# Performance work log

Measured on AMD Instinct MI355X. Metric: run time of the kernel, lower is better.

The kernel has to match this reference:

```python
import jax, jax.numpy as jnp
import numpy as np

B, T, C = 2, 4096, 768
N_HEAD = 12
HEAD_DIM = C // N_HEAD


def setup_inputs() -> dict:
    key = jax.random.key(0)
    k1, k2, k3, k4, k5 = jax.random.split(key, 5)
    scale = 1.0 / np.sqrt(C)
    x = jax.random.normal(k1, (B, T, C), dtype=jnp.float32)
    # weights stored as [in, out] (transpose of torch Linear weight)
    W_attn = jax.random.normal(k2, (C, 3 * C), dtype=jnp.float32) * scale
    b_attn = jax.random.normal(k3, (3 * C,), dtype=jnp.float32) * 0.01
    W_proj = jax.random.normal(k4, (C, C), dtype=jnp.float32) * scale
    b_proj = jax.random.normal(k5, (C,), dtype=jnp.float32) * 0.01
    return {"x": x, "W_attn": W_attn, "b_attn": b_attn, "W_proj": W_proj, "b_proj": b_proj}


def reference(x, W_attn, b_attn, W_proj, b_proj):
    Bq, Tq, Cq = x.shape
    qkv = x @ W_attn + b_attn                      # [B, T, 3C]
    q, k, v = jnp.split(qkv, 3, axis=-1)           # each [B, T, C]

    def heads(t):
        return t.reshape(Bq, Tq, N_HEAD, HEAD_DIM).transpose(0, 2, 1, 3)  # [B, H, T, D]

    q, k, v = heads(q), heads(k), heads(v)
    att = jnp.einsum('bhqd,bhkd->bhqk', q, k) * (1.0 / np.sqrt(HEAD_DIM))  # [B, H, T, T]
    causal = jnp.tril(jnp.ones((Tq, Tq), dtype=bool))                      # [T, T]
    att = jnp.where(causal[None, None], att, jnp.finfo(att.dtype).min)
    att = jax.nn.softmax(att, axis=-1)
    y = jnp.einsum('bhqk,bhkd->bhqd', att, v)      # [B, H, T, D]
    y = y.transpose(0, 2, 1, 3).reshape(Bq, Tq, Cq)
    return y @ W_proj + b_proj
```

## Files before the change

kernel.cpp:

```cpp
#include <hip/hip_runtime.h>


#define TSEQ   4096
#define NHEAD  12
#define CDIM   768
#define C3     2304
#define BT_TOT 8192

typedef __bf16 bf16x8 __attribute__((ext_vector_type(8)));
typedef __bf16 bf16x2 __attribute__((ext_vector_type(2)));
typedef float  f32x4  __attribute__((ext_vector_type(4)));
typedef unsigned int u32x4 __attribute__((ext_vector_type(4)));

__device__ __forceinline__ unsigned short f2bf(float f) {
  unsigned int u = __builtin_bit_cast(unsigned int, f);
  u += 0x7FFFu + ((u >> 16) & 1u);
  return (unsigned short)(u >> 16);
}

__device__ __forceinline__ unsigned int pack2bf(float a, float b) {
  bf16x2 v = {(__bf16)a, (__bf16)b};
  return __builtin_bit_cast(unsigned int, v);
}

__device__ __forceinline__ f32x4 mfma16(bf16x8 a, bf16x8 b, f32x4 c) {
  return __builtin_amdgcn_mfma_f32_16x16x32_bf16(a, b, c, 0, 0, 0);
}

typedef const __attribute__((address_space(1))) void* gas_ptr;
typedef __attribute__((address_space(3))) void* las_ptr;

#define WAIT_VM4() __builtin_amdgcn_s_waitcnt(0x3F74)
#define WAIT_VM0() __builtin_amdgcn_s_waitcnt(0x3F70)
#define SBAR()     __builtin_amdgcn_sched_barrier(0)


#define PREP_CAST_BLOCKS  6144
#define PREP_WA_BLOCKS    1728
#define PREP_WP_BLOCKS     576

__global__ __launch_bounds__(256) void prep_kernel(
    const float* __restrict__ x, unsigned short* __restrict__ xb,
    const float* __restrict__ W_attn, unsigned short* __restrict__ WaT,
    const float* __restrict__ W_proj, unsigned short* __restrict__ WpT) {
  const int bk = blockIdx.x;
  if (bk < PREP_CAST_BLOCKS) {
    int i = (bk * 256 + threadIdx.x) * 4;
    float4 v = *(const float4*)(x + i);
    ushort4 u;
    u.x = f2bf(v.x); u.y = f2bf(v.y); u.z = f2bf(v.z); u.w = f2bf(v.w);
    *(ushort4*)(xb + i) = u;
    return;
  }
  __shared__ float tile[32][33];
  const float* src;
  unsigned short* dst;
  int K, N, n0, k0;
  if (bk < PREP_CAST_BLOCKS + PREP_WA_BLOCKS) {
    const int j = bk - PREP_CAST_BLOCKS;
    src = W_attn; dst = WaT; K = CDIM; N = C3;
    n0 = (j % 72) * 32; k0 = (j / 72) * 32;
  } else {
    const int j = bk - (PREP_CAST_BLOCKS + PREP_WA_BLOCKS);
    src = W_proj; dst = WpT; K = CDIM; N = CDIM;
    n0 = (j % 24) * 32; k0 = (j / 24) * 32;
  }
  const int tx = threadIdx.x & 31, ty = threadIdx.x >> 5;
#pragma unroll
  for (int i = 0; i < 4; ++i)
    tile[ty + i * 8][tx] = src[(size_t)(k0 + ty + i * 8) * N + n0 + tx];
  __syncthreads();
#pragma unroll
  for (int i = 0; i < 4; ++i)
    dst[(size_t)(n0 + ty + i * 8) * K + k0 + tx] = f2bf(tile[tx][ty + i * 8]);
}


__device__ __forceinline__ void stage_gemm(const unsigned short* __restrict__ A,
                                           const unsigned short* __restrict__ BTm,
                                           int K, int m0, int n0, int k0,
                                           unsigned short* buf, int wave,
                                           int srow, int scol) {
#pragma unroll
  for (int r = 0; r < 2; ++r) {
    const unsigned short* ga = A + (size_t)(m0 + r * 64 + srow) * K + k0 + scol;
    __builtin_amdgcn_global_load_lds((gas_ptr)ga,
        (las_ptr)(buf + r * 2048 + wave * 512), 16, 0, 0);
    const unsigned short* gb = BTm + (size_t)(n0 + r * 64 + srow) * K + k0 + scol;
    __builtin_amdgcn_global_load_lds((gas_ptr)gb,
        (las_ptr)(buf + 4096 + r * 2048 + wave * 512), 16, 0, 0);
  }
}

__device__ __forceinline__ void gemm_bt_mainloop(const unsigned short* __restrict__ A,
                                                 const unsigned short* __restrict__ BTm,
                                                 int K, int m0, int n0,
                                                 unsigned short* lds, f32x4 acc[4][4]) {
  const int tid = threadIdx.x;
  const int wave = tid >> 6, lane = tid & 63;
  const int quad = lane >> 4, l16 = lane & 15;
  const int wm = (wave >> 1) * 64, wn = (wave & 1) * 64;
  const int srow = tid >> 2;
  const int scol = (tid & 3) * 8;

  const int nt = K / 32;
  stage_gemm(A, BTm, K, m0, n0, 0,  lds,        wave, srow, scol);
  stage_gemm(A, BTm, K, m0, n0, 32, lds + 8192, wave, srow, scol);
  WAIT_VM4();
  SBAR();
  __builtin_amdgcn_s_barrier();
  SBAR();

  for (int t = 0; t < nt; ++t) {
    if (t + 2 < nt) {
      stage_gemm(A, BTm, K, m0, n0, (t + 2) * 32, lds + ((t + 2) % 3) * 8192,
                 wave, srow, scol);
      WAIT_VM4();
    } else {
      WAIT_VM0();
    }
    SBAR();

    const unsigned short* buf = lds + (t % 3) * 8192;
    bf16x8 af[4], bfr[4];
#pragma unroll
    for (int i = 0; i < 4; ++i) {
      af[i]  = *(const bf16x8*)(buf + (wm + i * 16 + l16) * 32 + quad * 8);
      bfr[i] = *(const bf16x8*)(buf + 4096 + (wn + i * 16 + l16) * 32 + quad * 8);
    }
#pragma unroll
    for (int i = 0; i < 4; ++i)
#pragma unroll
      for (int j = 0; j < 4; ++j)
        acc[i][j] = mfma16(af[i], bfr[j], acc[i][j]);

    if (t + 1 < nt) {
      SBAR();
      __builtin_amdgcn_s_barrier();
      SBAR();
    }
  }
  __syncthreads();
}

__global__ __launch_bounds__(256, 3) void gemm_qkv_kernel(
    const unsigned short* __restrict__ A, const unsigned short* __restrict__ BTm,
    const float* __restrict__ bias,
    unsigned short* __restrict__ qbuf, unsigned short* __restrict__ kbuf,
    unsigned short* __restrict__ vtbuf) {
  __shared__ __align__(16) unsigned short lds[3 * 8192];
  f32x4 zero = {0.f, 0.f, 0.f, 0.f};
  f32x4 acc[4][4];
#pragma unroll
  for (int i = 0; i < 4; ++i)
#pragma unroll
    for (int j = 0; j < 4; ++j) acc[i][j] = zero;

  const int m0 = blockIdx.y * 128, n0 = blockIdx.x * 128;
  gemm_bt_mainloop(A, BTm, CDIM, m0, n0, lds, acc);

  const int tid = threadIdx.x;
  const int wave = tid >> 6, lane = tid & 63;
  const int quad = lane >> 4, l16 = lane & 15;
  const int wm = (wave >> 1) * 64, wn = (wave & 1) * 64;
  const float KSCALE = 0.125f * 1.44269504088896340736f;

  const int seg = n0 / CDIM;
  const float mult = (seg == 1) ? KSCALE : 1.0f;

#pragma unroll
  for (int j = 0; j < 4; ++j) {
    const int nl = wn + j * 16 + l16;
    const float bv = bias[n0 + nl];
#pragma unroll
    for (int i = 0; i < 4; ++i) {
#pragma unroll
      for (int r = 0; r < 4; ++r) {
        const int ml = wm + i * 16 + quad * 4 + r;
        unsigned short val = f2bf((acc[i][j][r] + bv) * mult);
        if (seg < 2) lds[ml * 136 + nl] = val;
        else         lds[nl * 136 + ml] = val;
      }
    }
  }
  __syncthreads();

  const int row = tid >> 1, half = tid & 1;
  const unsigned short* src = lds + row * 136 + half * 64;
  if (seg < 2) {
    const int m = m0 + row, b = m >> 12, t = m & (TSEQ - 1);
    const int nn = (n0 - seg * CDIM) + half * 64;
    const int h = nn >> 6;
    unsigned short* base = (seg == 0) ? qbuf : kbuf;
    unsigned short* dst = base + ((size_t)(b * NHEAD + h) * TSEQ + t) * 64;
#pragma unroll
    for (int k = 0; k < 8; ++k)
      *(uint4*)(dst + k * 8) = *(const uint4*)(src + k * 8);
  } else {
    const int nn = (n0 - 2 * CDIM) + row;
    const int h = nn >> 6, d = nn & 63;
    const int b = m0 >> 12, t0 = (m0 & (TSEQ - 1)) + half * 64;
    unsigned short* dst = vtbuf + ((size_t)(b * NHEAD + h) * 64 + d) * TSEQ + t0;
#pragma unroll
    for (int k = 0; k < 8; ++k) {
      const int s0 = 32 * (k >> 2) + 4 * (k & 3);
      uint2 a = *(const uint2*)(src + s0);
      uint2 c = *(const uint2*)(src + s0 + 16);
      uint4 w = {a.x, a.y, c.x, c.y};
      *(uint4*)(dst + k * 8) = w;
    }
  }
}

__global__ __launch_bounds__(256, 3) void gemm_out_kernel(
    const unsigned short* __restrict__ A, const unsigned short* __restrict__ BTm,
    const float* __restrict__ bias, float* __restrict__ out) {
  __shared__ __align__(16) unsigned short lds[3 * 8192];
  f32x4 zero = {0.f, 0.f, 0.f, 0.f};
  f32x4 acc[4][4];
#pragma unroll
  for (int i = 0; i < 4; ++i)
#pragma unroll
    for (int j = 0; j < 4; ++j) acc[i][j] = zero;

  const int m0 = blockIdx.y * 128, n0 = blockIdx.x * 128;
  gemm_bt_mainloop(A, BTm, CDIM, m0, n0, lds, acc);

  const int tid = threadIdx.x;
  const int wave = tid >> 6, lane = tid & 63;
  const int quad = lane >> 4, l16 = lane & 15;
  const int wm = (wave >> 1) * 64, wn = (wave & 1) * 64;

#pragma unroll
  for (int j = 0; j < 4; ++j) {
    int n = n0 + wn + j * 16 + l16;
    float bv = bias[n];
#pragma unroll
    for (int i = 0; i < 4; ++i) {
#pragma unroll
      for (int r = 0; r < 4; ++r) {
        int m = m0 + wm + i * 16 + quad * 4 + r;
        out[(size_t)m * CDIM + n] = acc[i][j][r] + bv;
      }
    }
  }
}


__device__ __forceinline__ void stage_kv(const unsigned short* __restrict__ Kp,
                                         const unsigned short* __restrict__ Vp,
                                         int j0, unsigned short* kb, unsigned short* vb,
                                         int tid, int wave) {
  const int row = tid >> 3;
  const int col = ((tid & 7) ^ (row & 7)) * 8;
  __builtin_amdgcn_global_load_lds((gas_ptr)(Kp + (size_t)(j0 + row) * 64 + col),
                                   (las_ptr)(kb + wave * 512), 16, 0, 0);
  __builtin_amdgcn_global_load_lds((gas_ptr)(Vp + (size_t)row * TSEQ + j0 + col),
                                   (las_ptr)(vb + wave * 512), 16, 0, 0);
}

__device__ __forceinline__ void qk_score(const bf16x8 kf[8], const bf16x8 qf[2], f32x4 s[4]) {
  f32x4 zero = {0.f, 0.f, 0.f, 0.f};
#pragma unroll
  for (int i = 0; i < 4; ++i)
    s[i] = mfma16(kf[2 * i + 1], qf[1], mfma16(kf[2 * i], qf[0], zero));
}

template <bool MASKED>
__device__ __forceinline__ void exp_pack(const f32x4 s[4], int j0, int qabs,
                                         int l16, int quad, float& lsum, bf16x8 pf[2]) {
  unsigned int w[8];
#pragma unroll
  for (int i = 0; i < 4; ++i) {
    float p[4];
#pragma unroll
    for (int r = 0; r < 4; ++r) {
      p[r] = __builtin_amdgcn_exp2f(s[i][r]);
      if (MASKED) {
        if (j0 + i * 16 + quad * 4 + r > qabs) p[r] = 0.f;
      }
      lsum += p[r];
    }
    w[2 * i]     = pack2bf(p[0], p[1]);
    w[2 * i + 1] = pack2bf(p[2], p[3]);
  }
  u32x4 lo = {w[0], w[1], w[2], w[3]};
  u32x4 hi = {w[4], w[5], w[6], w[7]};
  pf[0] = __builtin_bit_cast(bf16x8, lo);
  pf[1] = __builtin_bit_cast(bf16x8, hi);
}

__device__ __forceinline__ void pv(const unsigned short* __restrict__ vb,
                                   int l16, int quad, int x7,
                                   const bf16x8 pf[2], f32x4 o[4]) {
#pragma unroll
  for (int dt = 0; dt < 4; ++dt) {
    const unsigned short* vr = vb + (dt * 16 + l16) * 64;
    bf16x8 v0 = *(const bf16x8*)(vr + ((quad ^ x7) * 8));
    bf16x8 v1 = *(const bf16x8*)(vr + (((4 + quad) ^ x7) * 8));
    o[dt] = mfma16(v1, pf[1], mfma16(v0, pf[0], o[dt]));
  }
}

__global__ __launch_bounds__(512, 6) void attn_kernel(const unsigned short* __restrict__ qbuf,
                                                      const unsigned short* __restrict__ kbuf,
                                                      const unsigned short* __restrict__ vtbuf,
                                                      unsigned short* __restrict__ y) {
  __shared__ __align__(16) unsigned short k_lds[2][64 * 64];
  __shared__ __align__(16) unsigned short v_lds[2][64 * 64];

  const int tid = threadIdx.x;
  const int wave = tid >> 6, lane = tid & 63;
  const int quad = lane >> 4, l16 = lane & 15;
  const int x7 = l16 & 7;

  const int bh = blockIdx.x % 24;
  const int p = blockIdx.x / 24;
  const bool isA = wave < 4;
  const int qtile = isA ? p : (63 - p);
  const int q0 = qtile * 64 + (wave & 3) * 16;

  const unsigned short* Qp = qbuf + (size_t)bh * TSEQ * 64;
  const unsigned short* Kp = kbuf + (size_t)bh * TSEQ * 64;
  const unsigned short* Vp = vtbuf + (size_t)bh * 64 * TSEQ;

  bf16x8 qf[2];
  qf[0] = *(const bf16x8*)(Qp + (size_t)(q0 + l16) * 64 + quad * 8);
  qf[1] = *(const bf16x8*)(Qp + (size_t)(q0 + l16) * 64 + 32 + quad * 8);

  f32x4 zero = {0.f, 0.f, 0.f, 0.f};
  f32x4 o[4];
#pragma unroll
  for (int dt = 0; dt < 4; ++dt) o[dt] = zero;
  float ls = 0.f;

  const int kcol0 = (quad ^ x7) * 8;
  const int ntiles = 64 - p;
  const int lasttile = isA ? p : (ntiles - 1);

  stage_kv(Kp, Vp, 0, k_lds[0], v_lds[0], tid, wave);

  for (int jt = 0; jt < ntiles; ++jt) {
    __syncthreads();
    if (jt + 1 < ntiles)
      stage_kv(Kp, Vp, (jt + 1) * 64, k_lds[(jt + 1) & 1], v_lds[(jt + 1) & 1], tid, wave);

    if (jt <= lasttile) {
      const unsigned short* kb = k_lds[jt & 1];
      const unsigned short* vb = v_lds[jt & 1];
      const int j0 = jt * 64;

      bf16x8 kf[8];
#pragma unroll
      for (int i = 0; i < 4; ++i) {
        kf[2 * i]     = *(const bf16x8*)(kb + (16 * i + l16) * 64 + kcol0);
        kf[2 * i + 1] = *(const bf16x8*)(kb + (16 * i + l16) * 64 + (kcol0 ^ 32));
      }

      f32x4 s[4];
      qk_score(kf, qf, s);

      bf16x8 pf[2];
      if (jt == lasttile) exp_pack<true>(s, j0, q0 + l16, l16, quad, ls, pf);
      else                exp_pack<false>(s, j0, q0 + l16, l16, quad, ls, pf);

      pv(vb, l16, quad, x7, pf, o);
    }
  }

  ls += __shfl_xor(ls, 16); ls += __shfl_xor(ls, 32);
  const float inv = 1.0f / ls;

  const int b = bh / NHEAD, hd = bh - b * NHEAD;
  unsigned short* yr = y + (size_t)(b * TSEQ + q0 + l16) * CDIM + hd * 64 + quad * 4;
#pragma unroll
  for (int dt = 0; dt < 4; ++dt) {
    uint2 w;
    w.x = pack2bf(o[dt][0] * inv, o[dt][1] * inv);
    w.y = pack2bf(o[dt][2] * inv, o[dt][3] * inv);
    *(uint2*)(yr + dt * 16) = w;
  }
}


extern "C" void kernel_launch(void* const* d_in, const int* in_sizes, int n_in,
                              void* d_out, int out_size, void* d_ws, size_t ws_size,
                              hipStream_t stream) {
  const float* x      = (const float*)d_in[0];
  const float* W_attn = (const float*)d_in[1];
  const float* b_attn = (const float*)d_in[2];
  const float* W_proj = (const float*)d_in[3];
  const float* b_proj = (const float*)d_in[4];
  float* out = (float*)d_out;

  unsigned short* xb    = (unsigned short*)d_ws;
  unsigned short* WaT   = xb + (size_t)BT_TOT * CDIM;
  unsigned short* WpT   = WaT + (size_t)C3 * CDIM;
  unsigned short* qbuf  = WpT + (size_t)CDIM * CDIM;
  unsigned short* kbuf  = qbuf + (size_t)2 * NHEAD * TSEQ * 64;
  unsigned short* vtbuf = kbuf + (size_t)2 * NHEAD * TSEQ * 64;
  unsigned short* ybuf  = xb;

  prep_kernel<<<PREP_CAST_BLOCKS + PREP_WA_BLOCKS + PREP_WP_BLOCKS, 256, 0, stream>>>(
      x, xb, W_attn, WaT, W_proj, WpT);
  gemm_qkv_kernel<<<dim3(C3 / 128, BT_TOT / 128), 256, 0, stream>>>(xb, WaT, b_attn,
                                                                    qbuf, kbuf, vtbuf);
  attn_kernel<<<dim3(24 * 32), 512, 0, stream>>>(qbuf, kbuf, vtbuf, ybuf);
  gemm_out_kernel<<<dim3(CDIM / 128, BT_TOT / 128), 256, 0, stream>>>(ybuf, WpT, b_proj, out);
}
```

Before: 221.0 us.

## Use 64x128 tiles with a dedicated triple-buffered pipeline in output projection GEMM

```diff
diff --git a/kernel.cpp b/kernel.cpp
--- a/kernel.cpp
+++ b/kernel.cpp
@@ -31,6 +31,7 @@
 typedef __attribute__((address_space(3))) void* las_ptr;
 
 #define WAIT_VM4() __builtin_amdgcn_s_waitcnt(0x3F74)
+#define WAIT_VM3() __builtin_amdgcn_s_waitcnt(0x3F73)
 #define WAIT_VM0() __builtin_amdgcn_s_waitcnt(0x3F70)
 #define SBAR()     __builtin_amdgcn_sched_barrier(0)
 
@@ -212,31 +213,87 @@
   }
 }
 
-__global__ __launch_bounds__(256, 3) void gemm_out_kernel(
+
+__device__ __forceinline__ void stage_out(const unsigned short* __restrict__ A,
+                                          const unsigned short* __restrict__ BTm,
+                                          int m0, int n0, int k0,
+                                          unsigned short* buf, int wave,
+                                          int srow, int scol) {
+  const unsigned short* ga = A + (size_t)(m0 + srow) * CDIM + k0 + scol;
+  __builtin_amdgcn_global_load_lds((gas_ptr)ga,
+      (las_ptr)(buf + wave * 512), 16, 0, 0);
+#pragma unroll
+  for (int r = 0; r < 2; ++r) {
+    const unsigned short* gb = BTm + (size_t)(n0 + r * 64 + srow) * CDIM + k0 + scol;
+    __builtin_amdgcn_global_load_lds((gas_ptr)gb,
+        (las_ptr)(buf + 2048 + r * 2048 + wave * 512), 16, 0, 0);
+  }
+}
+
+__global__ __launch_bounds__(256, 4) void gemm_out_kernel(
     const unsigned short* __restrict__ A, const unsigned short* __restrict__ BTm,
     const float* __restrict__ bias, float* __restrict__ out) {
-  __shared__ __align__(16) unsigned short lds[3 * 8192];
+  __shared__ __align__(16) unsigned short lds[3 * 6144];
   f32x4 zero = {0.f, 0.f, 0.f, 0.f};
-  f32x4 acc[4][4];
-#pragma unroll
-  for (int i = 0; i < 4; ++i)
+  f32x4 acc[2][4];
+#pragma unroll
+  for (int i = 0; i < 2; ++i)
 #pragma unroll
     for (int j = 0; j < 4; ++j) acc[i][j] = zero;
 
-  const int m0 = blockIdx.y * 128, n0 = blockIdx.x * 128;
-  gemm_bt_mainloop(A, BTm, CDIM, m0, n0, lds, acc);
-
+  const int m0 = blockIdx.y * 64, n0 = blockIdx.x * 128;
   const int tid = threadIdx.x;
   const int wave = tid >> 6, lane = tid & 63;
   const int quad = lane >> 4, l16 = lane & 15;
-  const int wm = (wave >> 1) * 64, wn = (wave & 1) * 64;
+  const int wm = (wave >> 1) * 32, wn = (wave & 1) * 64;
+  const int srow = tid >> 2;
+  const int scol = (tid & 3) * 8;
+
+  const int nt = CDIM / 32;
+  stage_out(A, BTm, m0, n0, 0,  lds,        wave, srow, scol);
+  stage_out(A, BTm, m0, n0, 32, lds + 6144, wave, srow, scol);
+  WAIT_VM3();
+  SBAR();
+  __builtin_amdgcn_s_barrier();
+  SBAR();
+
+  for (int t = 0; t < nt; ++t) {
+    if (t + 2 < nt) {
+      stage_out(A, BTm, m0, n0, (t + 2) * 32, lds + ((t + 2) % 3) * 6144,
+                wave, srow, scol);
+      WAIT_VM3();
+    } else {
+      WAIT_VM0();
+    }
+    SBAR();
+
+    const unsigned short* buf = lds + (t % 3) * 6144;
+    bf16x8 af[2], bfr[4];
+#pragma unroll
+    for (int i = 0; i < 2; ++i)
+      af[i] = *(const bf16x8*)(buf + (wm + i * 16 + l16) * 32 + quad * 8);
+#pragma unroll
+    for (int j = 0; j < 4; ++j)
+      bfr[j] = *(const bf16x8*)(buf + 2048 + (wn + j * 16 + l16) * 32 + quad * 8);
+#pragma unroll
+    for (int i = 0; i < 2; ++i)
+#pragma unroll
+      for (int j = 0; j < 4; ++j)
+        acc[i][j] = mfma16(af[i], bfr[j], acc[i][j]);
+
+    if (t + 1 < nt) {
+      SBAR();
+      __builtin_amdgcn_s_barrier();
+      SBAR();
+    }
+  }
 
 #pragma unroll
   for (int j = 0; j < 4; ++j) {
     int n = n0 + wn + j * 16 + l16;
     float bv = bias[n];
 #pragma unroll
-    for (int i = 0; i < 4; ++i) {
+    for (int i = 0; i < 2; ++i) {
 #pragma unroll
       for (int r = 0; r < 4; ++r) {
         int m = m0 + wm + i * 16 + quad * 4 + r;
@@ -406,5 +463,5 @@
   gemm_qkv_kernel<<<dim3(C3 / 128, BT_TOT / 128), 256, 0, stream>>>(xb, WaT, b_attn,
                                                                     qbuf, kbuf, vtbuf);
   attn_kernel<<<dim3(24 * 32), 512, 0, stream>>>(qbuf, kbuf, vtbuf, ybuf);
-  gemm_out_kernel<<<dim3(CDIM / 128, BT_TOT / 128), 256, 0, stream>>>(ybuf, WpT, b_proj, out);
-}
+  gemm_out_kernel<<<dim3(CDIM / 128, BT_TOT / 64), 256, 0, stream>>>(ybuf, WpT, b_proj, out);
+}
```

Result: slower. 231.0 us (+4.6%).
